# Kernel tuning notes

Hardware: AMD Instinct MI355X
Metric: run time of the kernel (lower is better)

## Reference

```python
import jax, jax.numpy as jnp
import numpy as np

SCALE = 0.02
EPS = 1e-5


def setup_inputs() -> dict:
    key = jax.random.key(0)
    ks = jax.random.split(key, 11)
    C = 256
    inp = {
        "x": jax.random.normal(ks[0], (64, C, 28, 28), dtype=jnp.float32),
        "w1": jax.random.normal(ks[1], (C, C, 3, 3), dtype=jnp.float32) * 0.05,
        "g1": jax.random.uniform(ks[2], (C,), dtype=jnp.float32, minval=0.5, maxval=1.5),
        "b1": jax.random.normal(ks[3], (C,), dtype=jnp.float32) * 0.1,
        "m1": jax.random.normal(ks[4], (C,), dtype=jnp.float32) * 0.1,
        "v1": jax.random.uniform(ks[5], (C,), dtype=jnp.float32, minval=0.5, maxval=1.5),
        "w2": jax.random.normal(ks[6], (C, C, 3, 3), dtype=jnp.float32) * 0.05,
        "g2": jax.random.uniform(ks[7], (C,), dtype=jnp.float32, minval=0.5, maxval=1.5),
        "b2": jax.random.normal(ks[8], (C,), dtype=jnp.float32) * 0.1,
        "m2": jax.random.normal(ks[9], (C,), dtype=jnp.float32) * 0.1,
        "v2": jax.random.uniform(ks[10], (C,), dtype=jnp.float32, minval=0.5, maxval=1.5),
    }
    return inp


def _bin_conv3x3(x, w, stride=1):
    # 1-bit weight conv: sign(w)*scale, straight-through estimator for grads.
    wb = w + jax.lax.stop_gradient(jnp.sign(w) - w)
    y = jax.lax.conv_general_dilated(
        x, wb,
        window_strides=(stride, stride),
        padding=[(1, 1), (1, 1)],
        dimension_numbers=("NCHW", "OIHW", "NCHW"),
    )
    return y * SCALE


def _bn(x, g, b, m, v):
    # eval-mode batchnorm with running stats
    inv = g * jax.lax.rsqrt(v + EPS)  # [C]
    return x * inv[None, :, None, None] + (b - m * inv)[None, :, None, None]


def reference(x, w1, g1, b1, m1, v1, w2, g2, b2, m2, v2):
    out = jax.nn.relu(_bn(_bin_conv3x3(x, w1, 1), g1, b1, m1, v1))
    out = _bn(_bin_conv3x3(out, w2, 1), g2, b2, m2, v2)
    return jax.nn.relu(out + x)
```

## Files before the change

kernel.cpp:

```cpp
#include <hip/hip_runtime.h>

#define EPS_F 1e-5f
#define SCALE_F 0.02f

using short8  = __attribute__((ext_vector_type(8))) short;
using floatx4 = __attribute__((ext_vector_type(4))) float;

__device__ __forceinline__ unsigned short f2bf(float f) {
  unsigned u = __float_as_uint(f);
  return (unsigned short)((u + 0x7fffu + ((u >> 16) & 1u)) >> 16);
}

__global__ void prep_w(const float* __restrict__ w1, const float* __restrict__ w2,
                       unsigned short* __restrict__ ap1, unsigned short* __restrict__ ap2,
                       const float* g1, const float* b1, const float* m1, const float* v1,
                       const float* g2, const float* b2, const float* m2, const float* v2,
                       float* bnp) {
  const float* __restrict__ w = blockIdx.y ? w2 : w1;
  unsigned short* __restrict__ ap = blockIdx.y ? ap2 : ap1;
  int t = blockIdx.x * 256 + threadIdx.x;
  int off = t >> 13;
  int c8  = (t >> 8) & 31;
  int co  = t & 255;
  const float* ws = w + (size_t)(co * 256 + c8 * 8) * 9 + off;
  short8 o;
#pragma unroll
  for (int j = 0; j < 8; ++j) {
    float v = ws[j * 9];
    o[j] = (v > 0.f) ? (short)0x3F80 : ((v < 0.f) ? (short)0xBF80 : (short)0);
  }
  *(short8*)(ap + (size_t)t * 8) = o;
  if (blockIdx.x == 0 && blockIdx.y == 0) {
    int c = threadIdx.x;
    float i1 = g1[c] * rsqrtf(v1[c] + EPS_F);
    bnp[c]       = SCALE_F * i1;
    bnp[256 + c] = b1[c] - m1[c] * i1;
    float i2 = g2[c] * rsqrtf(v2[c] + EPS_F);
    bnp[512 + c] = SCALE_F * i2;
    bnp[768 + c] = b2[c] - m2[c] * i2;
  }
}

__global__ void prep_x(const float* __restrict__ x, unsigned short* __restrict__ xb,
                       unsigned short* __restrict__ abuf) {
  int h = blockIdx.x;
  int n = blockIdx.y;
  int tid = threadIdx.x;
  const float* xs = x + ((size_t)n * 256 + tid) * 784 + h * 28;
  unsigned short* xd = xb + ((size_t)n * 900 + (h + 1) * 30 + 1) * 256 + tid;
#pragma unroll
  for (int p4 = 0; p4 < 7; ++p4) {
    floatx4 f = *(const floatx4*)(xs + p4 * 4);
#pragma unroll
    for (int k = 0; k < 4; ++k)
      xd[(size_t)(p4 * 4 + k) * 256] = f2bf(f[k]);
  }
  {
    int bufi = tid >> 7, side = (tid >> 6) & 1, c4 = tid & 63;
    unsigned short* bb = (bufi ? abuf : xb) + ((size_t)n * 900 + (h + 1) * 30 + side * 29) * 256;
    ushort4 z = {0, 0, 0, 0};
    *(ushort4*)(bb + c4 * 4) = z;
  }
  if (h == 0 || h == 27) {
    int row = (h == 0) ? 0 : 29;
    for (int u = tid; u < 3840; u += 256) {
      int bufi = u / 1920;
      int r    = u - bufi * 1920;
      int px   = r >> 6, c4 = r & 63;
      unsigned short* bb = (bufi ? abuf : xb) + ((size_t)n * 900 + row * 30 + px) * 256;
      ushort4 z = {0, 0, 0, 0};
      *(ushort4*)(bb + c4 * 4) = z;
    }
  }
}

template<int STAGE>
__global__ __launch_bounds__(256, 2) void bconv(
    const unsigned short* __restrict__ Bin,
    const unsigned short* __restrict__ Apack,
    const float* __restrict__ bnp,
    unsigned short* __restrict__ aout,
    const float* __restrict__ xres,
    float* __restrict__ out)
{
  __shared__ __align__(16) unsigned short smem[STAGE == 1 ? 29568 : 24576];

  const int tid  = threadIdx.x;
  const int lane = tid & 63;
  const int wv   = tid >> 6;
  const int quad = lane >> 4;
  const int l16  = lane & 15;

  int flat = blockIdx.y * 7 + blockIdx.x;
  int idx  = (flat & 7) * 56 + (flat >> 3);
  const int n     = idx / 7;
  const int spBlk = idx - n * 7;

  const int prow0 = 4 * spBlk;
  const unsigned short* bsrc = Bin + ((size_t)n * 900 + prow0 * 30) * 256;
  const int coW = wv * 64;

  int pxS[7];
#pragma unroll
  for (int s = 0; s < 7; ++s) {
    int lm = s * 16 + l16;
    int hl = lm / 28;
    int w  = lm - hl * 28;
    pxS[s] = hl * 30 + w;
  }

  int goff0, goff1, goff2, goff3, goff4, goff5;
  {
#define MKGOFF(dst, r) { int v = (r) * 256 + tid; int px = v >> 3; \
    if (px > 179) px = 179; int c = (v & 7) ^ (px & 7); dst = px * 256 + c * 8; }
    MKGOFF(goff0, 0) MKGOFF(goff1, 1) MKGOFF(goff2, 2)
    MKGOFF(goff3, 3) MKGOFF(goff4, 4) MKGOFF(goff5, 5)
#undef MKGOFF
  }

#define STAGE_CB(cbi, bufsel) { \
  unsigned short* lb = smem + (bufsel) * 12288 + wv * 512; \
  const unsigned short* gb = bsrc + (cbi) * 64; \
  __builtin_amdgcn_global_load_lds((const __attribute__((address_space(1))) void*)(gb + goff0), \
      (__attribute__((address_space(3))) void*)(lb + 0 * 2048), 16, 0, 0); \
  __builtin_amdgcn_global_load_lds((const __attribute__((address_space(1))) void*)(gb + goff1), \
      (__attribute__((address_space(3))) void*)(lb + 1 * 2048), 16, 0, 0); \
  __builtin_amdgcn_global_load_lds((const __attribute__((address_space(1))) void*)(gb + goff2), \
      (__attribute__((address_space(3))) void*)(lb + 2 * 2048), 16, 0, 0); \
  __builtin_amdgcn_global_load_lds((const __attribute__((address_space(1))) void*)(gb + goff3), \
      (__attribute__((address_space(3))) void*)(lb + 3 * 2048), 16, 0, 0); \
  __builtin_amdgcn_global_load_lds((const __attribute__((address_space(1))) void*)(gb + goff4), \
      (__attribute__((address_space(3))) void*)(lb + 4 * 2048), 16, 0, 0); \
  __builtin_amdgcn_global_load_lds((const __attribute__((address_space(1))) void*)(gb + goff5), \
      (__attribute__((address_space(3))) void*)(lb + 5 * 2048), 16, 0, 0); }

#define LOADA(d0, d1, d2, d3, t, half, CQ8) { \
  const unsigned short* p = Apack + ((size_t)(((t) * 32 + (CQ8) + (half) * 4) * 256 + coW + l16)) * 8; \
  d0 = *(const short8*)p; \
  d1 = *(const short8*)(p + 128); \
  d2 = *(const short8*)(p + 256); \
  d3 = *(const short8*)(p + 384); }

#define HALFMMA(a0, a1, a2, a3, Cx, Dv) { \
  __builtin_amdgcn_s_setprio(1); \
  _Pragma("unroll") \
  for (int s = 0; s < 7; ++s) { \
    int pe = pxS[s] + (Dv); \
    short8 b = *(const short8*)&Blds[(pe << 6) + (((Cx) ^ (pe & 7)) << 3)]; \
    acc[0][s] = __builtin_amdgcn_mfma_f32_16x16x32_bf16(a0, b, acc[0][s], 0, 0, 0); \
    acc[1][s] = __builtin_amdgcn_mfma_f32_16x16x32_bf16(a1, b, acc[1][s], 0, 0, 0); \
    acc[2][s] = __builtin_amdgcn_mfma_f32_16x16x32_bf16(a2, b, acc[2][s], 0, 0, 0); \
    acc[3][s] = __builtin_amdgcn_mfma_f32_16x16x32_bf16(a3, b, acc[3][s], 0, 0, 0); \
  } \
  __builtin_amdgcn_s_setprio(0); }

  floatx4 acc[4][7];
#pragma unroll
  for (int c = 0; c < 4; ++c)
#pragma unroll
    for (int s = 0; s < 7; ++s)
      acc[c][s] = (floatx4){0.f, 0.f, 0.f, 0.f};

  short8 A0, A1, A2, A3, N0, N1, N2, N3;

  STAGE_CB(0, 0);
  LOADA(A0, A1, A2, A3, 0, 0, quad);
  LOADA(N0, N1, N2, N3, 0, 1, quad);
  __syncthreads();

#pragma unroll 1
  for (int cb = 0; cb < 4; ++cb) {
    unsigned short* Blds = smem + (cb & 1) * 12288;
    if (cb < 3) STAGE_CB(cb + 1, (cb + 1) & 1);
    const int cq8 = cb * 8 + quad;
    int D = 0;
#pragma unroll 1
    for (int t = 0; t < 9; ++t) {
      HALFMMA(A0, A1, A2, A3, quad, D);
      if (t < 8) LOADA(A0, A1, A2, A3, t + 1, 0, cq8);
      HALFMMA(N0, N1, N2, N3, 4 + quad, D);
      if (t < 8) LOADA(N0, N1, N2, N3, t + 1, 1, cq8);
      D += (t == 2 || t == 5) ? 28 : 1;
    }
    if (cb < 3) {
      LOADA(A0, A1, A2, A3, 0, 0, cq8 + 8);
      LOADA(N0, N1, N2, N3, 0, 1, cq8 + 8);
      __syncthreads();
    }
  }

  if (STAGE == 1) {
    __syncthreads();
#pragma unroll
    for (int c = 0; c < 4; ++c) {
      int co = coW + c * 16 + quad * 4;
      floatx4 As = *(const floatx4*)(bnp + co);
      floatx4 Bs = *(const floatx4*)(bnp + 256 + co);
#pragma unroll
      for (int s = 0; s < 7; ++s) {
        int px = s * 16 + l16;
        ushort4 o;
        o.x = f2bf(fmaxf(acc[c][s][0] * As[0] + Bs[0], 0.f));
        o.y = f2bf(fmaxf(acc[c][s][1] * As[1] + Bs[1], 0.f));
        o.z = f2bf(fmaxf(acc[c][s][2] * As[2] + Bs[2], 0.f));
        o.w = f2bf(fmaxf(acc[c][s][3] * As[3] + Bs[3], 0.f));
        *(ushort4*)&smem[px * 264 + co] = o;
      }
    }
    __syncthreads();
    unsigned short* dst0 = aout + ((size_t)n * 900 + (prow0 + 1) * 30 + 1) * 256;
    for (int u = tid; u < 3584; u += 256) {
      int px = u >> 5;
      int c8 = (u & 31) * 8;
      int r  = px / 28;
      int w  = px - r * 28;
      *(short8*)(dst0 + (size_t)(r * 30 + w) * 256 + c8) = *(const short8*)&smem[px * 264 + c8];
    }
  } else {
#pragma unroll
    for (int c = 0; c < 4; ++c) {
      int co = coW + c * 16 + quad * 4;
      floatx4 As = *(const floatx4*)(bnp + 512 + co);
      floatx4 Bs = *(const floatx4*)(bnp + 768 + co);
#pragma unroll
      for (int s = 0; s < 7; ++s) {
        int m = spBlk * 112 + s * 16 + l16;
#pragma unroll
        for (int r = 0; r < 4; ++r) {
          size_t oidx = ((size_t)n * 256 + co + r) * 784 + m;
          float v = acc[c][s][r] * As[r] + Bs[r] + xres[oidx];
          out[oidx] = fmaxf(v, 0.f);
        }
      }
    }
  }
#undef STAGE_CB
#undef LOADA
#undef HALFMMA
}


extern "C" void kernel_launch(void* const* d_in, const int* in_sizes, int n_in,
                              void* d_out, int out_size, void* d_ws, size_t ws_size,
                              hipStream_t stream) {
  const float* x  = (const float*)d_in[0];
  const float* w1 = (const float*)d_in[1];
  const float* g1 = (const float*)d_in[2];
  const float* b1 = (const float*)d_in[3];
  const float* m1 = (const float*)d_in[4];
  const float* v1 = (const float*)d_in[5];
  const float* w2 = (const float*)d_in[6];
  const float* g2 = (const float*)d_in[7];
  const float* b2 = (const float*)d_in[8];
  const float* m2 = (const float*)d_in[9];
  const float* v2 = (const float*)d_in[10];
  float* out = (float*)d_out;

  char* ws = (char*)d_ws;
  const size_t PADBUF = (size_t)64 * 900 * 256 * 2;
  const size_t WPACK  = 589824ull * 2;
  unsigned short* xb   = (unsigned short*)ws;
  unsigned short* abuf = (unsigned short*)(ws + PADBUF);
  unsigned short* ap1  = (unsigned short*)(ws + 2 * PADBUF);
  unsigned short* ap2  = (unsigned short*)(ws + 2 * PADBUF + WPACK);
  float* bnp           = (float*)(ws + 2 * PADBUF + 2 * WPACK);

  prep_w<<<dim3(288, 2), 256, 0, stream>>>(w1, w2, ap1, ap2,
                                           g1, b1, m1, v1, g2, b2, m2, v2, bnp);
  prep_x<<<dim3(28, 64), 256, 0, stream>>>(x, xb, abuf);

  dim3 grid(7, 64);
  bconv<1><<<grid, 256, 0, stream>>>(xb,   ap1, bnp, abuf, nullptr, nullptr);
  bconv<2><<<grid, 256, 0, stream>>>(abuf, ap2, bnp, nullptr, x, out);
}
```

Before: 230.7 us.

## Split conv output channels across two blocks and merge prep kernels

Each conv block now computes 128 output channels instead of 256, doubling the grid from 448 to 896 blocks and halving accumulators per wave. Launch bounds rise to 3 blocks per SM and the stage-1 LDS staging buffer shrinks. The two preprocessing kernels are merged into one launch to save a launch. The cost is that each block stages the same input tile, so B-operand loads into LDS are duplicated across the two channel halves, and each B fragment is reused by fewer MFMAs.

```diff
diff --git a/kernel.cpp b/kernel.cpp
--- a/kernel.cpp
+++ b/kernel.cpp
@@ -11,71 +11,76 @@
   return (unsigned short)((u + 0x7fffu + ((u >> 16) & 1u)) >> 16);
 }
 
-__global__ void prep_w(const float* __restrict__ w1, const float* __restrict__ w2,
-                       unsigned short* __restrict__ ap1, unsigned short* __restrict__ ap2,
-                       const float* g1, const float* b1, const float* m1, const float* v1,
-                       const float* g2, const float* b2, const float* m2, const float* v2,
-                       float* bnp) {
-  const float* __restrict__ w = blockIdx.y ? w2 : w1;
-  unsigned short* __restrict__ ap = blockIdx.y ? ap2 : ap1;
-  int t = blockIdx.x * 256 + threadIdx.x;
-  int off = t >> 13;
-  int c8  = (t >> 8) & 31;
-  int co  = t & 255;
-  const float* ws = w + (size_t)(co * 256 + c8 * 8) * 9 + off;
-  short8 o;
-#pragma unroll
-  for (int j = 0; j < 8; ++j) {
-    float v = ws[j * 9];
-    o[j] = (v > 0.f) ? (short)0x3F80 : ((v < 0.f) ? (short)0xBF80 : (short)0);
-  }
-  *(short8*)(ap + (size_t)t * 8) = o;
-  if (blockIdx.x == 0 && blockIdx.y == 0) {
-    int c = threadIdx.x;
-    float i1 = g1[c] * rsqrtf(v1[c] + EPS_F);
-    bnp[c]       = SCALE_F * i1;
-    bnp[256 + c] = b1[c] - m1[c] * i1;
-    float i2 = g2[c] * rsqrtf(v2[c] + EPS_F);
-    bnp[512 + c] = SCALE_F * i2;
-    bnp[768 + c] = b2[c] - m2[c] * i2;
-  }
-}
-
-__global__ void prep_x(const float* __restrict__ x, unsigned short* __restrict__ xb,
-                       unsigned short* __restrict__ abuf) {
-  int h = blockIdx.x;
-  int n = blockIdx.y;
+__global__ void prep_all(const float* __restrict__ w1, const float* __restrict__ w2,
+                         unsigned short* __restrict__ ap1, unsigned short* __restrict__ ap2,
+                         const float* g1, const float* b1, const float* m1, const float* v1,
+                         const float* g2, const float* b2, const float* m2, const float* v2,
+                         float* bnp,
+                         const float* __restrict__ x, unsigned short* __restrict__ xb,
+                         unsigned short* __restrict__ abuf) {
+  int bx = blockIdx.x;
   int tid = threadIdx.x;
-  const float* xs = x + ((size_t)n * 256 + tid) * 784 + h * 28;
-  unsigned short* xd = xb + ((size_t)n * 900 + (h + 1) * 30 + 1) * 256 + tid;
-#pragma unroll
-  for (int p4 = 0; p4 < 7; ++p4) {
-    floatx4 f = *(const floatx4*)(xs + p4 * 4);
-#pragma unroll
-    for (int k = 0; k < 4; ++k)
-      xd[(size_t)(p4 * 4 + k) * 256] = f2bf(f[k]);
-  }
-  {
-    int bufi = tid >> 7, side = (tid >> 6) & 1, c4 = tid & 63;
-    unsigned short* bb = (bufi ? abuf : xb) + ((size_t)n * 900 + (h + 1) * 30 + side * 29) * 256;
-    ushort4 z = {0, 0, 0, 0};
-    *(ushort4*)(bb + c4 * 4) = z;
-  }
-  if (h == 0 || h == 27) {
-    int row = (h == 0) ? 0 : 29;
-    for (int u = tid; u < 3840; u += 256) {
-      int bufi = u / 1920;
-      int r    = u - bufi * 1920;
-      int px   = r >> 6, c4 = r & 63;
-      unsigned short* bb = (bufi ? abuf : xb) + ((size_t)n * 900 + row * 30 + px) * 256;
+  if (bx < 576) {
+    int sel = bx >= 288;
+    int wx  = bx - sel * 288;
+    const float* __restrict__ w = sel ? w2 : w1;
+    unsigned short* __restrict__ ap = sel ? ap2 : ap1;
+    int t = wx * 256 + tid;
+    int off = t >> 13;
+    int c8  = (t >> 8) & 31;
+    int co  = t & 255;
+    const float* ws = w + (size_t)(co * 256 + c8 * 8) * 9 + off;
+    short8 o;
+#pragma unroll
+    for (int j = 0; j < 8; ++j) {
+      float v = ws[j * 9];
+      o[j] = (v > 0.f) ? (short)0x3F80 : ((v < 0.f) ? (short)0xBF80 : (short)0);
+    }
+    *(short8*)(ap + (size_t)t * 8) = o;
+    if (wx == 0 && sel == 0) {
+      int c = tid;
+      float i1 = g1[c] * rsqrtf(v1[c] + EPS_F);
+      bnp[c]       = SCALE_F * i1;
+      bnp[256 + c] = b1[c] - m1[c] * i1;
+      float i2 = g2[c] * rsqrtf(v2[c] + EPS_F);
+      bnp[512 + c] = SCALE_F * i2;
+      bnp[768 + c] = b2[c] - m2[c] * i2;
+    }
+  } else {
+    int p = bx - 576;
+    int h = p % 28;
+    int n = p / 28;
+    const float* xs = x + ((size_t)n * 256 + tid) * 784 + h * 28;
+    unsigned short* xd = xb + ((size_t)n * 900 + (h + 1) * 30 + 1) * 256 + tid;
+#pragma unroll
+    for (int p4 = 0; p4 < 7; ++p4) {
+      floatx4 f = *(const floatx4*)(xs + p4 * 4);
+#pragma unroll
+      for (int k = 0; k < 4; ++k)
+        xd[(size_t)(p4 * 4 + k) * 256] = f2bf(f[k]);
+    }
+    {
+      int bufi = tid >> 7, side = (tid >> 6) & 1, c4 = tid & 63;
+      unsigned short* bb = (bufi ? abuf : xb) + ((size_t)n * 900 + (h + 1) * 30 + side * 29) * 256;
       ushort4 z = {0, 0, 0, 0};
       *(ushort4*)(bb + c4 * 4) = z;
     }
+    if (h == 0 || h == 27) {
+      int row = (h == 0) ? 0 : 29;
+      for (int u = tid; u < 3840; u += 256) {
+        int bufi = u / 1920;
+        int r    = u - bufi * 1920;
+        int px   = r >> 6, c4 = r & 63;
+        unsigned short* bb = (bufi ? abuf : xb) + ((size_t)n * 900 + row * 30 + px) * 256;
+        ushort4 z = {0, 0, 0, 0};
+        *(ushort4*)(bb + c4 * 4) = z;
+      }
+    }
   }
 }
 
 template<int STAGE>
-__global__ __launch_bounds__(256, 2) void bconv(
+__global__ __launch_bounds__(256, 3) void bconv(
     const unsigned short* __restrict__ Bin,
     const unsigned short* __restrict__ Apack,
     const float* __restrict__ bnp,
@@ -83,7 +88,7 @@
     const float* __restrict__ xres,
     float* __restrict__ out)
 {
-  __shared__ __align__(16) unsigned short smem[STAGE == 1 ? 29568 : 24576];
+  __shared__ __align__(16) unsigned short smem[24576];
 
   const int tid  = threadIdx.x;
   const int lane = tid & 63;
@@ -91,14 +96,16 @@
   const int quad = lane >> 4;
   const int l16  = lane & 15;
 
-  int flat = blockIdx.y * 7 + blockIdx.x;
-  int idx  = (flat & 7) * 56 + (flat >> 3);
-  const int n     = idx / 7;
-  const int spBlk = idx - n * 7;
+  int flat = blockIdx.y * 14 + blockIdx.x;
+  int idx  = (flat & 7) * 112 + (flat >> 3);
+  const int n      = idx / 14;
+  const int rem    = idx - n * 14;
+  const int spBlk  = rem >> 1;
+  const int coHalf = rem & 1;
 
   const int prow0 = 4 * spBlk;
   const unsigned short* bsrc = Bin + ((size_t)n * 900 + prow0 * 30) * 256;
-  const int coW = wv * 64;
+  const int coW = coHalf * 128 + wv * 32;
 
   int pxS[7];
 #pragma unroll
@@ -134,14 +141,12 @@
   __builtin_amdgcn_global_load_lds((const __attribute__((address_space(1))) void*)(gb + goff5), \
       (__attribute__((address_space(3))) void*)(lb + 5 * 2048), 16, 0, 0); }
 
-#define LOADA(d0, d1, d2, d3, t, half, CQ8) { \
+#define LOADA2(d0, d1, t, half, CQ8) { \
   const unsigned short* p = Apack + ((size_t)(((t) * 32 + (CQ8) + (half) * 4) * 256 + coW + l16)) * 8; \
   d0 = *(const short8*)p; \
-  d1 = *(const short8*)(p + 128); \
-  d2 = *(const short8*)(p + 256); \
-  d3 = *(const short8*)(p + 384); }
-
-#define HALFMMA(a0, a1, a2, a3, Cx, Dv) { \
+  d1 = *(const short8*)(p + 128); }
+
+#define HALFMMA2(a0, a1, Cx, Dv) { \
   __builtin_amdgcn_s_setprio(1); \
   _Pragma("unroll") \
   for (int s = 0; s < 7; ++s) { \
@@ -149,23 +154,21 @@
     short8 b = *(const short8*)&Blds[(pe << 6) + (((Cx) ^ (pe & 7)) << 3)]; \
     acc[0][s] = __builtin_amdgcn_mfma_f32_16x16x32_bf16(a0, b, acc[0][s], 0, 0, 0); \
     acc[1][s] = __builtin_amdgcn_mfma_f32_16x16x32_bf16(a1, b, acc[1][s], 0, 0, 0); \
-    acc[2][s] = __builtin_amdgcn_mfma_f32_16x16x32_bf16(a2, b, acc[2][s], 0, 0, 0); \
-    acc[3][s] = __builtin_amdgcn_mfma_f32_16x16x32_bf16(a3, b, acc[3][s], 0, 0, 0); \
   } \
   __builtin_amdgcn_s_setprio(0); }
 
-  floatx4 acc[4][7];
-#pragma unroll
-  for (int c = 0; c < 4; ++c)
+  floatx4 acc[2][7];
+#pragma unroll
+  for (int c = 0; c < 2; ++c)
 #pragma unroll
     for (int s = 0; s < 7; ++s)
       acc[c][s] = (floatx4){0.f, 0.f, 0.f, 0.f};
 
-  short8 A0, A1, A2, A3, N0, N1, N2, N3;
+  short8 A0, A1, N0, N1;
 
   STAGE_CB(0, 0);
-  LOADA(A0, A1, A2, A3, 0, 0, quad);
-  LOADA(N0, N1, N2, N3, 0, 1, quad);
+  LOADA2(A0, A1, 0, 0, quad);
+  LOADA2(N0, N1, 0, 1, quad);
   __syncthreads();
 
 #pragma unroll 1
@@ -176,15 +179,15 @@
     int D = 0;
 #pragma unroll 1
     for (int t = 0; t < 9; ++t) {
-      HALFMMA(A0, A1, A2, A3, quad, D);
-      if (t < 8) LOADA(A0, A1, A2, A3, t + 1, 0, cq8);
-      HALFMMA(N0, N1, N2, N3, 4 + quad, D);
-      if (t < 8) LOADA(N0, N1, N2, N3, t + 1, 1, cq8);
+      HALFMMA2(A0, A1, quad, D);
+      if (t < 8) LOADA2(A0, A1, t + 1, 0, cq8);
+      HALFMMA2(N0, N1, 4 + quad, D);
+      if (t < 8) LOADA2(N0, N1, t + 1, 1, cq8);
       D += (t == 2 || t == 5) ? 28 : 1;
     }
     if (cb < 3) {
-      LOADA(A0, A1, A2, A3, 0, 0, cq8 + 8);
-      LOADA(N0, N1, N2, N3, 0, 1, cq8 + 8);
+      LOADA2(A0, A1, 0, 0, cq8 + 8);
+      LOADA2(N0, N1, 0, 1, cq8 + 8);
       __syncthreads();
     }
   }
@@ -192,8 +195,9 @@
   if (STAGE == 1) {
     __syncthreads();
 #pragma unroll
-    for (int c = 0; c < 4; ++c) {
-      int co = coW + c * 16 + quad * 4;
+    for (int c = 0; c < 2; ++c) {
+      int co  = coW + c * 16 + quad * 4;
+      int coL = (wv * 32) + c * 16 + quad * 4;
       floatx4 As = *(const floatx4*)(bnp + co);
       floatx4 Bs = *(const floatx4*)(bnp + 256 + co);
 #pragma unroll
@@ -204,21 +208,21 @@
         o.y = f2bf(fmaxf(acc[c][s][1] * As[1] + Bs[1], 0.f));
         o.z = f2bf(fmaxf(acc[c][s][2] * As[2] + Bs[2], 0.f));
         o.w = f2bf(fmaxf(acc[c][s][3] * As[3] + Bs[3], 0.f));
-        *(ushort4*)&smem[px * 264 + co] = o;
+        *(ushort4*)&smem[px * 136 + coL] = o;
       }
     }
     __syncthreads();
-    unsigned short* dst0 = aout + ((size_t)n * 900 + (prow0 + 1) * 30 + 1) * 256;
-    for (int u = tid; u < 3584; u += 256) {
-      int px = u >> 5;
-      int c8 = (u & 31) * 8;
+    unsigned short* dst0 = aout + ((size_t)n * 900 + (prow0 + 1) * 30 + 1) * 256 + coHalf * 128;
+    for (int u = tid; u < 1792; u += 256) {
+      int px = u >> 4;
+      int c8 = (u & 15) * 8;
       int r  = px / 28;
       int w  = px - r * 28;
-      *(short8*)(dst0 + (size_t)(r * 30 + w) * 256 + c8) = *(const short8*)&smem[px * 264 + c8];
+      *(short8*)(dst0 + (size_t)(r * 30 + w) * 256 + c8) = *(const short8*)&smem[px * 136 + c8];
     }
   } else {
 #pragma unroll
-    for (int c = 0; c < 4; ++c) {
+    for (int c = 0; c < 2; ++c) {
       int co = coW + c * 16 + quad * 4;
       floatx4 As = *(const floatx4*)(bnp + 512 + co);
       floatx4 Bs = *(const floatx4*)(bnp + 768 + co);
@@ -235,8 +239,8 @@
     }
   }
 #undef STAGE_CB
-#undef LOADA
-#undef HALFMMA
+#undef LOADA2
+#undef HALFMMA2
 }
 
 
@@ -265,11 +269,11 @@
   unsigned short* ap2  = (unsigned short*)(ws + 2 * PADBUF + WPACK);
   float* bnp           = (float*)(ws + 2 * PADBUF + 2 * WPACK);
 
-  prep_w<<<dim3(288, 2), 256, 0, stream>>>(w1, w2, ap1, ap2,
-                                           g1, b1, m1, v1, g2, b2, m2, v2, bnp);
-  prep_x<<<dim3(28, 64), 256, 0, stream>>>(x, xb, abuf);
-
-  dim3 grid(7, 64);
+  prep_all<<<dim3(2368), 256, 0, stream>>>(w1, w2, ap1, ap2,
+                                           g1, b1, m1, v1, g2, b2, m2, v2, bnp,
+                                           x, xb, abuf);
+
+  dim3 grid(14, 64);
   bconv<1><<<grid, 256, 0, stream>>>(xb,   ap1, bnp, abuf, nullptr, nullptr);
   bconv<2><<<grid, 256, 0, stream>>>(abuf, ap2, bnp, nullptr, x, out);
 }
```

Result: slower. 252.8 us (+9.6%).
